# Performance work log

Hardware: AMD Instinct MI355X
Metric: run time of the kernel (lower is better)

## Reference

```python
import jax, jax.numpy as jnp
import numpy as np

B, A, D = 512, 32, 256      # batch clips, actors (nodes per graph), feature dim
E = 1048576                 # total edges over the flattened (B*A)-node graph
THRESHOLD = 0.5             # config.knn.threshold
EPS = 1e-5


def setup_inputs() -> dict:
    key = jax.random.key(0)
    k1, k2, k3 = jax.random.split(key, 3)
    N = B * A
    X = jax.random.normal(k1, (B, A, D), dtype=jnp.float32)
    edge_index = jax.random.randint(k2, (2, E), 0, N, dtype=jnp.int32)
    W = jax.random.normal(k3, (D, D), dtype=jnp.float32) * (1.0 / np.sqrt(D))
    b = jnp.zeros((D,), dtype=jnp.float32)
    return {"X": X, "edge_index": edge_index, "W": W, "b": b}


def gcn_conv(x, edge_index, W, b):
    # Standard GCNConv: x' = D^-1/2 (A + I) D^-1/2 (x W) + b
    N = x.shape[0]
    x = x @ W                                            # [N, D]
    loop = jnp.arange(N, dtype=edge_index.dtype)
    src = jnp.concatenate([edge_index[0], loop])         # message sources
    tgt = jnp.concatenate([edge_index[1], loop])         # aggregation targets
    deg = jax.ops.segment_sum(jnp.ones_like(src, dtype=x.dtype), tgt,
                              num_segments=N)            # in-degree incl. self-loop
    dinv = jnp.where(deg > 0, jax.lax.rsqrt(deg), 0.0)
    coef = (dinv[src] * dinv[tgt])[:, None]              # symmetric norm per edge
    out = jax.ops.segment_sum(x[src] * coef, tgt, num_segments=N)
    return out + b


def reference(X, edge_index, W, b):
    Bq, Aq, Dq = X.shape
    x = X.reshape(Bq * Aq, Dq)
    x = gcn_conv(x, edge_index, W, b)
    Xo = x.reshape(Bq, Aq, Dq)

    # cal_edge: pairwise squared distances per batch, min-max normalized,
    # thresholded. Instead of variable-length dense_to_sparse edge lists we
    # return the equivalent fixed-shape adjacency mask [B, A, A].
    inner = -2.0 * jnp.einsum('bad,bcd->bac', Xo, Xo)
    sq = jnp.sum(Xo * Xo, axis=-1, keepdims=True)        # [B, A, 1]
    scores = sq + inner + jnp.swapaxes(sq, -1, -2)       # [B, A, A]
    smin = scores.min(axis=-1, keepdims=True)
    smax = scores.max(axis=-1, keepdims=True)
    scores = (scores - smin) / (smax - smin + EPS)
    adj_mask = scores > THRESHOLD                        # new edge set (dense form)
    return Xo, adj_mask
```

## Files before the change

### kernel.cpp

```cpp
#include <hip/hip_runtime.h>

#define BQ 512
#define AQ 32
#define DQ 256
#define NQ (BQ * AQ)
#define EQ 1048576
#define THR 0.5f
#define EPSF 1e-5f
#define DEG_STRIDE 160
#define BIN_TGTS 64
#define NBINS (NQ / BIN_TGTS)
#define BIN_STRIDE 4864

typedef __attribute__((ext_vector_type(8))) short bf16x8;
typedef __attribute__((ext_vector_type(4))) float f32x4;

__device__ __forceinline__ unsigned short f2bf(float f) {
    unsigned int u = __float_as_uint(f);
    return (unsigned short)((u + 0x7FFFu + ((u >> 16) & 1u)) >> 16);
}
__device__ __forceinline__ float bf2f(unsigned short h) {
    return __uint_as_float((unsigned int)h << 16);
}

__global__ __launch_bounds__(256) void k_wt_part(
        const float* __restrict__ W, unsigned short* __restrict__ Wt,
        const int* __restrict__ src, const int* __restrict__ tgt,
        int* __restrict__ bin_cursor, unsigned int* __restrict__ binned) {
    __shared__ int hist[NBINS];
    int tid = threadIdx.x;
    if (blockIdx.x < 256) {
        int idx = blockIdx.x * 256 + tid;
        int n = idx >> 8;
        int k = idx & 255;
        float w = W[k * DQ + n];
        unsigned short h = f2bf(w);
        Wt[idx] = h;
        Wt[DQ * DQ + idx] = f2bf(w - bf2f(h));
        return;
    }
    hist[tid] = 0;
    __syncthreads();
    int base = (blockIdx.x - 256) * 2048;
    int t[8], s[8];
    #pragma unroll
    for (int i = 0; i < 8; i++) {
        int e = base + i * 256 + tid;
        t[i] = tgt[e];
        s[i] = src[e];
        atomicAdd(&hist[t[i] >> 6], 1);
    }
    __syncthreads();
    int mine = hist[tid];
    __syncthreads();
    hist[tid] = tid * BIN_STRIDE + atomicAdd(&bin_cursor[tid], mine);
    __syncthreads();
    #pragma unroll
    for (int i = 0; i < 8; i++) {
        int slot = atomicAdd(&hist[t[i] >> 6], 1);
        binned[slot] = ((unsigned int)t[i] << 14) | (unsigned int)s[i];
    }
}

__global__ __launch_bounds__(256) void k_gemm_cnt(
        const float* __restrict__ Xp, const unsigned short* __restrict__ Wt,
        unsigned short* __restrict__ xwb,
        const int* __restrict__ bin_cursor, const unsigned int* __restrict__ binned,
        float* __restrict__ dinv) {
    __shared__ unsigned short bs[2][128 * 40];
    int tid = threadIdx.x;
    if (blockIdx.x >= 512) {
        int* lcnt = (int*)&bs[0][0];
        int b = blockIdx.x - 512;
        if (tid < BIN_TGTS) lcnt[tid] = 0;
        __syncthreads();
        int beg = b * BIN_STRIDE;
        int count = bin_cursor[b];
        if (count > BIN_STRIDE) count = BIN_STRIDE;
        for (int i = beg + tid; i < beg + count; i += 256) {
            unsigned int ed = binned[i];
            atomicAdd(&lcnt[(ed >> 14) & 63], 1);
        }
        __syncthreads();
        if (tid < BIN_TGTS)
            dinv[b * BIN_TGTS + tid] = rsqrtf((float)(lcnt[tid] + 1));
        return;
    }
    int mtile = blockIdx.x >> 1;
    int nbase = (blockIdx.x & 1) * 128;
    int wave = tid >> 6;
    int lane = tid & 63;
    int col = lane & 15;
    int quad = lane >> 4;
    int mbase = mtile * 64 + wave * 16;
    int m = mbase + col;

    const float* arow = Xp + (size_t)m * DQ;

    f32x4 acc[8];
    f32x4 zero = {0.f, 0.f, 0.f, 0.f};
    #pragma unroll
    for (int i = 0; i < 8; i++) acc[i] = zero;

    for (int k0 = 0; k0 < DQ; k0 += 32) {
        __syncthreads();
        {
            int row = tid & 127;
            int plane = tid >> 7;
            const uint4* g = (const uint4*)(Wt + (size_t)plane * DQ * DQ +
                                            (size_t)(nbase + row) * DQ + k0);
            uint4* l = (uint4*)&bs[plane][row * 40];
            #pragma unroll
            for (int u = 0; u < 4; u++) l[u] = g[u];
        }
        __syncthreads();

        int kq = k0 + quad * 8;
        float4 a0 = *(const float4*)(arow + kq);
        float4 a1 = *(const float4*)(arow + kq + 4);
        float av[8] = {a0.x, a0.y, a0.z, a0.w, a1.x, a1.y, a1.z, a1.w};
        bf16x8 ah, al;
        #pragma unroll
        for (int j = 0; j < 8; j++) {
            unsigned short h = f2bf(av[j]);
            ah[j] = (short)h;
            al[j] = (short)f2bf(av[j] - bf2f(h));
        }
        #pragma unroll
        for (int nt = 0; nt < 8; nt++) {
            int n = nt * 16 + col;
            bf16x8 bh = *(const bf16x8*)&bs[0][n * 40 + quad * 8];
            bf16x8 bl = *(const bf16x8*)&bs[1][n * 40 + quad * 8];
            acc[nt] = __builtin_amdgcn_mfma_f32_16x16x32_bf16(ah, bh, acc[nt], 0, 0, 0);
            acc[nt] = __builtin_amdgcn_mfma_f32_16x16x32_bf16(al, bh, acc[nt], 0, 0, 0);
            acc[nt] = __builtin_amdgcn_mfma_f32_16x16x32_bf16(ah, bl, acc[nt], 0, 0, 0);
        }
    }

    #pragma unroll
    for (int nt = 0; nt < 8; nt++) {
        #pragma unroll
        for (int r = 0; r < 4; r++) {
            xwb[(size_t)(mbase + quad * 4 + r) * DQ + nbase + nt * 16 + col] =
                f2bf(acc[nt][r]);
        }
    }
}

__global__ __launch_bounds__(512) void k_agg_scores(
        const unsigned int* __restrict__ xwb,
        const unsigned int* __restrict__ binned,
        const int* __restrict__ bin_cursor,
        const float* __restrict__ dinv,
        const float* __restrict__ bias,
        float* __restrict__ out,
        float* __restrict__ mask) {
    __shared__ float xs[AQ][DQ + 4];
    __shared__ float sq[AQ];
    __shared__ float sc[AQ][AQ + 1];
    __shared__ float rmin[AQ], rmax[AQ];
    __shared__ unsigned short lbuck[AQ * DEG_STRIDE];
    __shared__ int lcnt[AQ];

    int tid = threadIdx.x;
    int wave = tid >> 6;
    int lane = tid & 63;
    int bq = blockIdx.x;
    const uint2* xw2 = (const uint2*)xwb;

    if (tid < AQ) lcnt[tid] = 0;
    __syncthreads();
    {
        int b = bq >> 1;
        int beg = b * BIN_STRIDE;
        int count = bin_cursor[b];
        if (count > BIN_STRIDE) count = BIN_STRIDE;
        for (int i = beg + tid; i < beg + count; i += 512) {
            unsigned int ed = binned[i];
            if ((int)(ed >> 19) == bq) {
                int a = (ed >> 14) & 31;
                int pos = atomicAdd(&lcnt[a], 1);
                if (pos < DEG_STRIDE)
                    lbuck[a * DEG_STRIDE + pos] = (unsigned short)(ed & 0x3FFFu);
            }
        }
    }
    __syncthreads();

    float4 bv = ((const float4*)bias)[lane];

    #pragma unroll 1
    for (int i = 0; i < 4; i++) {
        int a = wave * 4 + i;
        int t = bq * AQ + a;
        float dt = dinv[t];
        float c0 = dt * dt;
        uint2 sp = xw2[(size_t)t * 64 + lane];
        float4 acc;
        acc.x = __uint_as_float(sp.x << 16) * c0;
        acc.y = __uint_as_float(sp.x & 0xFFFF0000u) * c0;
        acc.z = __uint_as_float(sp.y << 16) * c0;
        acc.w = __uint_as_float(sp.y & 0xFFFF0000u) * c0;

        int num = lcnt[a];
        if (num > DEG_STRIDE) num = DEG_STRIDE;
        for (int k0 = 0; k0 < num; k0 += 64) {
            int rem = num - k0;
            int n = rem < 64 ? rem : 64;
            int idx = k0 + (lane < n ? lane : 0);
            int e = (int)lbuck[a * DEG_STRIDE + idx];
            float cl = (lane < n) ? dinv[e] * dt : 0.f;
            int n8 = (n + 7) & ~7;
            for (int j0 = 0; j0 < n8; j0 += 8) {
                #pragma unroll
                for (int jj = 0; jj < 8; jj++) {
                    int j = j0 + jj;
                    int s = __shfl(e, j);
                    float c = __shfl(cl, j);
                    uint2 p = xw2[(size_t)s * 64 + lane];
                    acc.x += __uint_as_float(p.x << 16) * c;
                    acc.y += __uint_as_float(p.x & 0xFFFF0000u) * c;
                    acc.z += __uint_as_float(p.y << 16) * c;
                    acc.w += __uint_as_float(p.y & 0xFFFF0000u) * c;
                }
            }
        }

        acc.x += bv.x; acc.y += bv.y; acc.z += bv.z; acc.w += bv.w;
        ((float4*)out)[(size_t)t * 64 + lane] = acc;
        *(float4*)&xs[a][lane * 4] = acc;
    }
    __syncthreads();

    if (tid < AQ) {
        const float4* xi = (const float4*)xs[tid];
        float s = 0.f;
        #pragma unroll 8
        for (int dd = 0; dd < DQ / 4; dd++) {
            float4 a = xi[dd];
            s += a.x * a.x + a.y * a.y + a.z * a.z + a.w * a.w;
        }
        sq[tid] = s;
    }
    __syncthreads();

    {
        int p0 = tid * 2;
        int i = p0 >> 5;
        int j0 = p0 & 31;
        const float4* xi = (const float4*)xs[i];
        float g[2] = {0.f, 0.f};
        for (int dd = 0; dd < DQ / 4; dd += 8) {
            float4 ar[8];
            #pragma unroll
            for (int u = 0; u < 8; u++) ar[u] = xi[dd + u];
            #pragma unroll
            for (int q = 0; q < 2; q++) {
                const float4* xj = (const float4*)xs[j0 + q];
                float gq = 0.f;
                #pragma unroll
                for (int u = 0; u < 8; u++) {
                    float4 b = xj[dd + u];
                    gq += ar[u].x * b.x + ar[u].y * b.y +
                          ar[u].z * b.z + ar[u].w * b.w;
                }
                g[q] += gq;
            }
        }
        #pragma unroll
        for (int q = 0; q < 2; q++) {
            sc[i][j0 + q] = sq[i] - 2.f * g[q] + sq[j0 + q];
        }
    }
    __syncthreads();

    if (tid < AQ) {
        float mn = sc[tid][0], mx = sc[tid][0];
        for (int j = 1; j < AQ; j++) {
            float v = sc[tid][j];
            mn = fminf(mn, v);
            mx = fmaxf(mx, v);
        }
        rmin[tid] = mn;
        rmax[tid] = mx;
    }
    __syncthreads();

    {
        float* mb = mask + (size_t)bq * AQ * AQ;
        int p0 = tid * 2;
        int i = p0 >> 5, j0 = p0 & 31;
        float inv = 1.0f / (rmax[i] - rmin[i] + EPSF);
        float2 mv;
        mv.x = ((sc[i][j0 + 0] - rmin[i]) * inv > THR) ? 1.0f : 0.0f;
        mv.y = ((sc[i][j0 + 1] - rmin[i]) * inv > THR) ? 1.0f : 0.0f;
        ((float2*)mb)[tid] = mv;
    }
}

extern "C" void kernel_launch(void* const* d_in, const int* in_sizes, int n_in,
                              void* d_out, int out_size, void* d_ws, size_t ws_size,
                              hipStream_t stream) {
    const float* X    = (const float*)d_in[0];
    const int*   ei   = (const int*)d_in[1];
    const float* W    = (const float*)d_in[2];
    const float* bias = (const float*)d_in[3];
    float* out = (float*)d_out;

    char* ws = (char*)d_ws;
    unsigned short* xwb = (unsigned short*)ws;
    unsigned int* binned = (unsigned int*)(ws + (size_t)NQ * DQ * 2);
    unsigned short* Wt = (unsigned short*)(binned + (size_t)NBINS * BIN_STRIDE);
    float* dinv = (float*)(Wt + 2 * DQ * DQ);
    int* bin_cursor = (int*)(dinv + NQ);

    const int* src = ei;
    const int* tgt = ei + EQ;

    hipMemsetAsync(bin_cursor, 0, NBINS * sizeof(int), stream);
    k_wt_part<<<768, 256, 0, stream>>>(W, Wt, src, tgt, bin_cursor, binned);
    k_gemm_cnt<<<768, 256, 0, stream>>>(X, Wt, xwb, bin_cursor, binned, dinv);
    k_agg_scores<<<BQ, 512, 0, stream>>>((const unsigned int*)xwb, binned,
                                         bin_cursor, dinv, bias, out,
                                         out + (size_t)NQ * DQ);
}
```

Measured before the change: 174.1 us.

## Replace atomic edge binning with count-scan-scatter partitioning

Edge partitioning into target bins now runs as a deterministic three-phase counting sort. A per-block histogram is followed by a per-bin prefix scan, fused into the GEMM launch, and then a scatter using precomputed offsets. This removes the memset and the global atomic cursor contention, and the scatter results no longer depend on block arrival order. In exchange it adds two kernel launches, a second pass over the target array, and extra workspace for the count and base tables.

```diff
diff --git a/kernel.cpp b/kernel.cpp
--- a/kernel.cpp
+++ b/kernel.cpp
@@ -11,6 +11,8 @@
 #define BIN_TGTS 64
 #define NBINS (NQ / BIN_TGTS)
 #define BIN_STRIDE 4864
+#define NBLK_P 256
+#define EPB (EQ / NBLK_P)
 
 typedef __attribute__((ext_vector_type(8))) short bf16x8;
 typedef __attribute__((ext_vector_type(4))) float f32x4;
@@ -23,10 +25,9 @@
     return __uint_as_float((unsigned int)h << 16);
 }
 
-__global__ __launch_bounds__(256) void k_wt_part(
+__global__ __launch_bounds__(256) void k_wt_count(
         const float* __restrict__ W, unsigned short* __restrict__ Wt,
-        const int* __restrict__ src, const int* __restrict__ tgt,
-        int* __restrict__ bin_cursor, unsigned int* __restrict__ binned) {
+        const int* __restrict__ tgt, int* __restrict__ cntT) {
     __shared__ int hist[NBINS];
     int tid = threadIdx.x;
     if (blockIdx.x < 256) {
@@ -39,55 +40,47 @@
         Wt[DQ * DQ + idx] = f2bf(w - bf2f(h));
         return;
     }
+    int b = blockIdx.x - 256;
     hist[tid] = 0;
     __syncthreads();
-    int base = (blockIdx.x - 256) * 2048;
-    int t[8], s[8];
-    #pragma unroll
-    for (int i = 0; i < 8; i++) {
-        int e = base + i * 256 + tid;
-        t[i] = tgt[e];
-        s[i] = src[e];
-        atomicAdd(&hist[t[i] >> 6], 1);
-    }
-    __syncthreads();
-    int mine = hist[tid];
-    __syncthreads();
-    hist[tid] = tid * BIN_STRIDE + atomicAdd(&bin_cursor[tid], mine);
-    __syncthreads();
-    #pragma unroll
-    for (int i = 0; i < 8; i++) {
-        int slot = atomicAdd(&hist[t[i] >> 6], 1);
-        binned[slot] = ((unsigned int)t[i] << 14) | (unsigned int)s[i];
-    }
-}
-
-__global__ __launch_bounds__(256) void k_gemm_cnt(
+    int base = b * EPB;
+    #pragma unroll
+    for (int i = 0; i < 16; i++) {
+        int t = tgt[base + i * 256 + tid];
+        atomicAdd(&hist[t >> 6], 1);
+    }
+    __syncthreads();
+    cntT[tid * NBLK_P + b] = hist[tid];
+}
+
+__global__ __launch_bounds__(256) void k_scan_gemm(
         const float* __restrict__ Xp, const unsigned short* __restrict__ Wt,
         unsigned short* __restrict__ xwb,
-        const int* __restrict__ bin_cursor, const unsigned int* __restrict__ binned,
-        float* __restrict__ dinv) {
+        const int* __restrict__ cntT, int* __restrict__ baseT,
+        int* __restrict__ bin_cursor) {
     __shared__ unsigned short bs[2][128 * 40];
     int tid = threadIdx.x;
-    if (blockIdx.x >= 512) {
-        int* lcnt = (int*)&bs[0][0];
-        int b = blockIdx.x - 512;
-        if (tid < BIN_TGTS) lcnt[tid] = 0;
+    if (blockIdx.x < 256) {
+        int* sdat = (int*)&bs[0][0];
+        int b = blockIdx.x;
+        int v = cntT[b * NBLK_P + tid];
+        sdat[tid] = v;
         __syncthreads();
-        int beg = b * BIN_STRIDE;
-        int count = bin_cursor[b];
-        if (count > BIN_STRIDE) count = BIN_STRIDE;
-        for (int i = beg + tid; i < beg + count; i += 256) {
-            unsigned int ed = binned[i];
-            atomicAdd(&lcnt[(ed >> 14) & 63], 1);
-        }
-        __syncthreads();
-        if (tid < BIN_TGTS)
-            dinv[b * BIN_TGTS + tid] = rsqrtf((float)(lcnt[tid] + 1));
+        #pragma unroll
+        for (int off = 1; off < 256; off <<= 1) {
+            int add = (tid >= off) ? sdat[tid - off] : 0;
+            __syncthreads();
+            sdat[tid] += add;
+            __syncthreads();
+        }
+        int incl = sdat[tid];
+        baseT[b * NBLK_P + tid] = b * BIN_STRIDE + (incl - v);
+        if (tid == 255) bin_cursor[b] = incl;
         return;
     }
-    int mtile = blockIdx.x >> 1;
-    int nbase = (blockIdx.x & 1) * 128;
+    int bx = blockIdx.x - 256;
+    int mtile = bx >> 1;
+    int nbase = (bx & 1) * 128;
     int wave = tid >> 6;
     int lane = tid & 63;
     int col = lane & 15;
@@ -145,6 +138,49 @@
                 f2bf(acc[nt][r]);
         }
     }
+}
+
+__global__ __launch_bounds__(256) void k_scatter(
+        const int* __restrict__ src, const int* __restrict__ tgt,
+        const int* __restrict__ baseT, unsigned int* __restrict__ binned) {
+    __shared__ int lcur[NBINS];
+    int tid = threadIdx.x;
+    int b = blockIdx.x;
+    lcur[tid] = baseT[tid * NBLK_P + b];
+    __syncthreads();
+    int base = b * EPB;
+    int t[16], s[16];
+    #pragma unroll
+    for (int i = 0; i < 16; i++) {
+        int e = base + i * 256 + tid;
+        t[i] = tgt[e];
+        s[i] = src[e];
+    }
+    #pragma unroll
+    for (int i = 0; i < 16; i++) {
+        int slot = atomicAdd(&lcur[t[i] >> 6], 1);
+        binned[slot] = ((unsigned int)t[i] << 14) | (unsigned int)s[i];
+    }
+}
+
+__global__ __launch_bounds__(256) void k_cnt(
+        const int* __restrict__ bin_cursor, const unsigned int* __restrict__ binned,
+        float* __restrict__ dinv) {
+    __shared__ int lcnt[BIN_TGTS];
+    int tid = threadIdx.x;
+    int b = blockIdx.x;
+    if (tid < BIN_TGTS) lcnt[tid] = 0;
+    __syncthreads();
+    int beg = b * BIN_STRIDE;
+    int count = bin_cursor[b];
+    if (count > BIN_STRIDE) count = BIN_STRIDE;
+    for (int i = beg + tid; i < beg + count; i += 256) {
+        unsigned int ed = binned[i];
+        atomicAdd(&lcnt[(ed >> 14) & 63], 1);
+    }
+    __syncthreads();
+    if (tid < BIN_TGTS)
+        dinv[b * BIN_TGTS + tid] = rsqrtf((float)(lcnt[tid] + 1));
 }
 
 __global__ __launch_bounds__(512) void k_agg_scores(
@@ -313,13 +349,16 @@
     unsigned short* Wt = (unsigned short*)(binned + (size_t)NBINS * BIN_STRIDE);
     float* dinv = (float*)(Wt + 2 * DQ * DQ);
     int* bin_cursor = (int*)(dinv + NQ);
+    int* cntT = bin_cursor + NBINS;
+    int* baseT = cntT + NBINS * NBLK_P;
 
     const int* src = ei;
     const int* tgt = ei + EQ;
 
-    hipMemsetAsync(bin_cursor, 0, NBINS * sizeof(int), stream);
-    k_wt_part<<<768, 256, 0, stream>>>(W, Wt, src, tgt, bin_cursor, binned);
-    k_gemm_cnt<<<768, 256, 0, stream>>>(X, Wt, xwb, bin_cursor, binned, dinv);
+    k_wt_count<<<512, 256, 0, stream>>>(W, Wt, tgt, cntT);
+    k_scan_gemm<<<768, 256, 0, stream>>>(X, Wt, xwb, cntT, baseT, bin_cursor);
+    k_scatter<<<NBLK_P, 256, 0, stream>>>(src, tgt, baseT, binned);
+    k_cnt<<<256, 256, 0, stream>>>(bin_cursor, binned, dinv);
     k_agg_scores<<<BQ, 512, 0, stream>>>((const unsigned int*)xwb, binned,
                                          bin_cursor, dinv, bias, out,
                                          out + (size_t)NQ * DQ);
```

Measured after the change: 173.6 us. About the same (-0.3%).
